# Performance work log

Hardware: AMD Instinct MI355X
Metric: run time of the kernel (lower is better)

## Reference

```python
import jax, jax.numpy as jnp
import numpy as np

TOPK = 6
E = 512
IN = 384
M = 8192
LN_EPS = 1e-5


def _lin(x, w, b):
    # torch nn.Linear: y = x @ W^T + b, W is [out, in]
    return x @ w.T + b


def setup_inputs() -> dict:
    key = jax.random.key(0)
    ks = jax.random.split(key, 16)
    s = lambda k, sh: (jax.random.normal(k, sh, dtype=jnp.float32) * 0.02)
    return {
        "x": jax.random.normal(ks[0], (1, M, IN), dtype=jnp.float32),
        "fc1_w": s(ks[1], (E, IN)), "fc1_b": jnp.zeros((E,), jnp.float32),
        "wh_w": s(ks[2], (E, E)),   "wh_b": jnp.zeros((E,), jnp.float32),
        "wt_w": s(ks[3], (E, E)),   "wt_b": jnp.zeros((E,), jnp.float32),
        "l1_w": s(ks[4], (E, E)),   "l1_b": jnp.zeros((E,), jnp.float32),
        "l2_w": s(ks[5], (E, E)),   "l2_b": jnp.zeros((E,), jnp.float32),
        "a1_w": s(ks[6], (E // 2, E)), "a1_b": jnp.zeros((E // 2,), jnp.float32),
        "a2_w": s(ks[7], (1, E // 2)), "a2_b": jnp.zeros((1,), jnp.float32),
        "ln_g": jnp.ones((E,), jnp.float32), "ln_b": jnp.zeros((E,), jnp.float32),
    }


def reference(x, fc1_w, fc1_b, wh_w, wh_b, wt_w, wt_b,
              l1_w, l1_b, l2_w, l2_b, a1_w, a1_b, a2_w, a2_b, ln_g, ln_b):
    lrelu = jax.nn.leaky_relu  # slope 0.01 == torch default
    h = lrelu(_lin(x, fc1_w, fc1_b))                      # [B,M,E]
    h = (h + h.mean(axis=1, keepdims=True)) * 0.5
    e_h = _lin(h, wh_w, wh_b)                             # [B,M,E]
    e_t = _lin(h, wt_w, wt_b)                             # [B,M,E]
    scale = E ** (-0.5)
    attn_logit = (e_h * scale) @ jnp.swapaxes(e_t, -2, -1)  # [B,M,M]
    topk_weight, topk_index = jax.lax.top_k(attn_logit, TOPK)  # [B,M,K]
    # gather top-k neighbor tail embeddings: [B,M,K,E]
    Nb_h = jax.vmap(lambda et, idx: et[idx])(e_t, topk_index)
    topk_prob = jax.nn.softmax(topk_weight, axis=2)       # [B,M,K]
    eh_r = topk_prob[..., None] * Nb_h + (1.0 - topk_prob)[..., None] * e_h[:, :, None, :]
    gate = jnp.tanh(e_h[:, :, None, :] + eh_r)            # [B,M,K,E]
    # faithful to torch einsum('ijkl,ijkm->ijk'): sums l and m independently
    ka_weight = Nb_h.sum(axis=-1) * gate.sum(axis=-1)     # [B,M,K]
    ka_prob = jax.nn.softmax(ka_weight, axis=2)           # [B,M,K]
    e_Nh = jnp.einsum('bmk,bmke->bme', ka_prob, Nb_h)     # [B,M,E]
    sum_emb = lrelu(_lin(e_h + e_Nh, l1_w, l1_b))
    bi_emb = lrelu(_lin(e_h * e_Nh, l2_w, l2_b))
    emb = sum_emb + bi_emb                                # [B,M,E] (dropout = eval identity)
    hn = emb[0]                                           # squeeze(0) -> [M,E]
    # GeoGlobalAttention readout: gate_nn = Linear->LeakyReLU->Linear, softmax over nodes
    g = _lin(lrelu(_lin(hn, a1_w, a1_b)), a2_w, a2_b)     # [M,1]
    att = jax.nn.softmax(g, axis=0)
    pooled = (att * hn).sum(axis=0, keepdims=True)        # [1,E]
    mu = pooled.mean(axis=-1, keepdims=True)
    var = jnp.mean((pooled - mu) ** 2, axis=-1, keepdims=True)
    out = (pooled - mu) / jnp.sqrt(var + LN_EPS) * ln_g + ln_b
    return out
```

## Files before the change

kernel.cpp:

```cpp
#include <hip/hip_runtime.h>
#include <math.h>
#include <stdint.h>

#define M_NODES 8192
#define E_DIM   512
#define NTOPK   6
#define ATTN_SCALE 0.04419417382415922f
#define NEG_BIG (-1e38f)
#define CAND_CAP 192

typedef __attribute__((ext_vector_type(8))) short short8;
typedef __attribute__((ext_vector_type(4))) float f32x4;

__device__ __forceinline__ float lrelu(float v) { return v > 0.f ? v : 0.01f * v; }

__device__ __forceinline__ unsigned short f2bf(float f) {
  uint32_t u = __float_as_uint(f);
  uint32_t r = (u + 0x7FFFu + ((u >> 16) & 1u)) >> 16;
  return (unsigned short)r;
}
__device__ __forceinline__ float bf2f(unsigned short s) {
  return __uint_as_float(((uint32_t)s) << 16);
}

__device__ __forceinline__ void async_cp16(const void* gptr, void* lds) {
  auto g1 = reinterpret_cast<const __attribute__((address_space(1))) unsigned int*>(
      reinterpret_cast<uintptr_t>(gptr));
  auto l3 = reinterpret_cast<__attribute__((address_space(3))) unsigned int*>(
      reinterpret_cast<uintptr_t>(lds));
  __builtin_amdgcn_global_load_lds(g1, l3, 16, 0, 0);
}



__global__ __launch_bounds__(256) void wcast_kernel(
    const float* __restrict__ x, const float* __restrict__ fc1w,
    const float* __restrict__ whw, const float* __restrict__ wtw,
    const float* __restrict__ l1w, const float* __restrict__ l2w,
    const float* __restrict__ a1w,
    unsigned short* __restrict__ xT, unsigned short* __restrict__ fc1T,
    unsigned short* __restrict__ whT, unsigned short* __restrict__ wtT,
    unsigned short* __restrict__ l1T, unsigned short* __restrict__ l2T,
    unsigned short* __restrict__ a1T)
{
  const int gid = blockIdx.x * 256 + threadIdx.x;
  const float* src; unsigned short* dst; int K8, local;
  if (gid < 417792) {
    K8 = 48;
    if (gid < 393216) { src = x; dst = xT; local = gid; }
    else { src = fc1w; dst = fc1T; local = gid - 393216; }
  } else {
    K8 = 64;
    if (gid < 450560)      { src = whw; dst = whT; local = gid - 417792; }
    else if (gid < 483328) { src = wtw; dst = wtT; local = gid - 450560; }
    else if (gid < 516096) { src = l1w; dst = l1T; local = gid - 483328; }
    else if (gid < 548864) { src = l2w; dst = l2T; local = gid - 516096; }
    else                   { src = a1w; dst = a1T; local = gid - 548864; }
  }
  const int m = local / K8;
  const int k8 = local - m * K8;
  const float* p = src + (size_t)m * (K8 * 8) + k8 * 8;
  float4 v0 = ((const float4*)p)[0];
  float4 v1 = ((const float4*)p)[1];
  const int Kt = K8 >> 2;
  const size_t ti = ((size_t)(m >> 4) * Kt + (k8 >> 2)) * 512 + ((m & 15) + 16 * (k8 & 3)) * 8;
  uint4 pk;
  pk.x = (uint32_t)f2bf(v0.x) | ((uint32_t)f2bf(v0.y) << 16);
  pk.y = (uint32_t)f2bf(v0.z) | ((uint32_t)f2bf(v0.w) << 16);
  pk.z = (uint32_t)f2bf(v1.x) | ((uint32_t)f2bf(v1.y) << 16);
  pk.w = (uint32_t)f2bf(v1.z) | ((uint32_t)f2bf(v1.w) << 16);
  *(uint4*)(dst + ti) = pk;
}

template <int MODE>
__global__ __launch_bounds__(256) void mfma_gemm(
    const unsigned short* __restrict__ At1, const unsigned short* __restrict__ At2,
    const unsigned short* __restrict__ Wt1, const unsigned short* __restrict__ Wt2,
    const float* __restrict__ b1, const float* __restrict__ b2,
    float* __restrict__ Cf, unsigned short* __restrict__ T1,
    unsigned short* __restrict__ T2, unsigned short* __restrict__ Cbf,
    unsigned short* __restrict__ Cbf2, int N, int K)
{
  constexpr bool DUALW = (MODE == 1 || MODE == 2);
  __shared__ unsigned short As[2][8 * 512];
  __shared__ unsigned short Bs[2][4 * 512];
  const int Kt = K >> 5;
  const int tid = threadIdx.x, lane = tid & 63, w = tid >> 6;
  const int m0 = blockIdx.y * 128, n0 = blockIdx.x * 64;

  f32x4 acc0[2][4], acc1[2][4];
#pragma unroll
  for (int p = 0; p < 2; p++)
#pragma unroll
    for (int j = 0; j < 4; j++) {
      acc0[p][j] = (f32x4){0.f, 0.f, 0.f, 0.f};
      acc1[p][j] = (f32x4){0.f, 0.f, 0.f, 0.f};
    }

  for (int kt = 0; kt < Kt; kt++) {
    const unsigned short* a1p = At1 + ((size_t)((m0 >> 4) + 2 * w) * Kt + kt) * 512 + lane * 8;
    async_cp16(a1p, &As[0][(2 * w) * 512]);
    async_cp16(a1p + (size_t)Kt * 512, &As[0][(2 * w + 1) * 512]);
    if (MODE == 2) {
      const unsigned short* a2p = At2 + ((size_t)((m0 >> 4) + 2 * w) * Kt + kt) * 512 + lane * 8;
      async_cp16(a2p, &As[1][(2 * w) * 512]);
      async_cp16(a2p + (size_t)Kt * 512, &As[1][(2 * w + 1) * 512]);
    }
    const unsigned short* bp1 = Wt1 + ((size_t)((n0 >> 4) + w) * Kt + kt) * 512 + lane * 8;
    async_cp16(bp1, &Bs[0][w * 512]);
    if (DUALW) {
      const unsigned short* bp2 = Wt2 + ((size_t)((n0 >> 4) + w) * Kt + kt) * 512 + lane * 8;
      async_cp16(bp2, &Bs[1][w * 512]);
    }
    __syncthreads();
    short8 a[2], a2[2], bb[4], bb2[4];
#pragma unroll
    for (int p = 0; p < 2; p++) a[p] = *(const short8*)&As[0][(2 * w + p) * 512 + lane * 8];
    if (MODE == 2) {
#pragma unroll
      for (int p = 0; p < 2; p++) a2[p] = *(const short8*)&As[1][(2 * w + p) * 512 + lane * 8];
    }
#pragma unroll
    for (int j = 0; j < 4; j++) bb[j] = *(const short8*)&Bs[0][j * 512 + lane * 8];
    if (DUALW) {
#pragma unroll
      for (int j = 0; j < 4; j++) bb2[j] = *(const short8*)&Bs[1][j * 512 + lane * 8];
    }
#pragma unroll
    for (int p = 0; p < 2; p++)
#pragma unroll
      for (int j = 0; j < 4; j++) {
        acc0[p][j] = __builtin_amdgcn_mfma_f32_16x16x32_bf16(a[p], bb[j], acc0[p][j], 0, 0, 0);
        if (MODE == 1)
          acc1[p][j] = __builtin_amdgcn_mfma_f32_16x16x32_bf16(a[p], bb2[j], acc1[p][j], 0, 0, 0);
        if (MODE == 2)
          acc1[p][j] = __builtin_amdgcn_mfma_f32_16x16x32_bf16(a2[p], bb2[j], acc1[p][j], 0, 0, 0);
      }
    __syncthreads();
  }

  const int lrow = (lane >> 4) * 4, lcol = lane & 15;

  if (MODE == 3) {
    float part[2][4] = {};
#pragma unroll
    for (int p = 0; p < 2; p++)
#pragma unroll
      for (int j = 0; j < 4; j++) {
        const int c = n0 + j * 16 + lcol;
        const float bias1 = b1[c];
        const float w2 = b2[c];
#pragma unroll
        for (int d = 0; d < 4; d++)
          part[p][d] = fmaf(lrelu(acc0[p][j][d] + bias1), w2, part[p][d]);
      }
#pragma unroll
    for (int p = 0; p < 2; p++)
#pragma unroll
      for (int d = 0; d < 4; d++) {
#pragma unroll
        for (int off = 1; off < 16; off <<= 1)
          part[p][d] += __shfl_xor(part[p][d], off);
      }
    if (lcol == 0) {
#pragma unroll
      for (int p = 0; p < 2; p++)
#pragma unroll
        for (int d = 0; d < 4; d++)
          atomicAdd(&Cf[m0 + w * 32 + p * 16 + lrow + d], part[p][d]);
    }
    return;
  }

  if (MODE == 4) {
    float colp[4] = {};
#pragma unroll
    for (int p = 0; p < 2; p++)
#pragma unroll
      for (int j = 0; j < 4; j++) {
        const int c = n0 + j * 16 + lcol;
        const float bias1 = b1[c];
#pragma unroll
        for (int d = 0; d < 4; d++) {
          const int r = m0 + w * 32 + p * 16 + lrow + d;
          const float v = lrelu(acc0[p][j][d] + bias1);
          Cbf[(size_t)r * N + c] = f2bf(v);
          colp[j] += v;
        }
      }
#pragma unroll
    for (int j = 0; j < 4; j++) {
      colp[j] += __shfl_xor(colp[j], 16);
      colp[j] += __shfl_xor(colp[j], 32);
    }
    if (lane < 16) {
#pragma unroll
      for (int j = 0; j < 4; j++)
        atomicAdd(&Cf[n0 + j * 16 + lcol], colp[j]);
    }
    return;
  }

  const int NT = N >> 5;
#pragma unroll
  for (int p = 0; p < 2; p++)
#pragma unroll
    for (int j = 0; j < 4; j++) {
      const int c = n0 + j * 16 + lcol;
      const float bias1 = b1[c];
      const float bias2 = DUALW ? b2[c] : 0.f;
#pragma unroll
      for (int d = 0; d < 4; d++) {
        const int r = m0 + w * 32 + p * 16 + lrow + d;
        const float v0 = acc0[p][j][d] + bias1;
        const size_t ti = ((size_t)(r >> 4) * NT + (c >> 5)) * 512 +
                          ((r & 15) + 16 * ((c >> 3) & 3)) * 8 + (c & 7);
        if (MODE == 1) {
          const float v1 = acc1[p][j][d] + bias2;
          T1[ti] = f2bf(v0);
          T2[ti] = f2bf(v1);
          Cbf[(size_t)r * N + c] = f2bf(v0);
          Cbf2[(size_t)r * N + c] = f2bf(v1);
        } else {
          const float e = lrelu(v0) + lrelu(acc1[p][j][d] + bias2);
          T1[ti] = f2bf(e);
          Cbf[(size_t)r * N + c] = f2bf(e);
        }
      }
    }
}

__global__ __launch_bounds__(256) void hupd_cast_kernel(
    const unsigned short* __restrict__ hRow, const float* __restrict__ colsum,
    unsigned short* __restrict__ hT)
{
  const int gid = blockIdx.x * 256 + threadIdx.x;
  const int m = gid >> 6, k8 = gid & 63;
  short8 hv = *(const short8*)(hRow + (size_t)m * E_DIM + k8 * 8);
  float4 c0 = *(const float4*)(colsum + k8 * 8);
  float4 c1 = *(const float4*)(colsum + k8 * 8 + 4);
  const float im = 1.f / (float)M_NODES;
  float v[8];
#pragma unroll
  for (int e = 0; e < 8; e++) v[e] = bf2f((unsigned short)hv[e]);
  v[0] = (v[0] + c0.x * im) * 0.5f; v[1] = (v[1] + c0.y * im) * 0.5f;
  v[2] = (v[2] + c0.z * im) * 0.5f; v[3] = (v[3] + c0.w * im) * 0.5f;
  v[4] = (v[4] + c1.x * im) * 0.5f; v[5] = (v[5] + c1.y * im) * 0.5f;
  v[6] = (v[6] + c1.z * im) * 0.5f; v[7] = (v[7] + c1.w * im) * 0.5f;
  const size_t ti = ((size_t)(m >> 4) * 16 + (k8 >> 2)) * 512 + ((m & 15) + 16 * (k8 & 3)) * 8;
  uint4 pk;
  pk.x = (uint32_t)f2bf(v[0]) | ((uint32_t)f2bf(v[1]) << 16);
  pk.y = (uint32_t)f2bf(v[2]) | ((uint32_t)f2bf(v[3]) << 16);
  pk.z = (uint32_t)f2bf(v[4]) | ((uint32_t)f2bf(v[5]) << 16);
  pk.w = (uint32_t)f2bf(v[6]) | ((uint32_t)f2bf(v[7]) << 16);
  *(uint4*)(hT + ti) = pk;
}

__global__ __launch_bounds__(256, 4) void sgemm_kernel(
    const unsigned short* __restrict__ ehT, const unsigned short* __restrict__ etT,
    unsigned short* __restrict__ sc, float* __restrict__ tmax)
{
  __shared__ unsigned short As[8 * 512];
  __shared__ unsigned short Bs[8 * 512];
  const int tid = threadIdx.x, lane = tid & 63, w = tid >> 6;
  const int wr = w >> 1, wc = w & 1;
  const int m0 = blockIdx.y * 128;
  const int n0 = blockIdx.x * 128;

  f32x4 acc[4][4];
#pragma unroll
  for (int i = 0; i < 4; i++)
#pragma unroll
    for (int j = 0; j < 4; j++) acc[i][j] = (f32x4){0.f, 0.f, 0.f, 0.f};

  for (int kt = 0; kt < 16; kt++) {
    const int s0 = w, s1 = w + 4;
    async_cp16(ehT + ((size_t)((m0 >> 4) + s0) * 16 + kt) * 512 + lane * 8, &As[s0 * 512]);
    async_cp16(ehT + ((size_t)((m0 >> 4) + s1) * 16 + kt) * 512 + lane * 8, &As[s1 * 512]);
    async_cp16(etT + ((size_t)((n0 >> 4) + s0) * 16 + kt) * 512 + lane * 8, &Bs[s0 * 512]);
    async_cp16(etT + ((size_t)((n0 >> 4) + s1) * 16 + kt) * 512 + lane * 8, &Bs[s1 * 512]);
    __syncthreads();
    short8 a[4], b[4];
#pragma unroll
    for (int i = 0; i < 4; i++) a[i] = *(const short8*)&As[(wr * 4 + i) * 512 + lane * 8];
#pragma unroll
    for (int j = 0; j < 4; j++) b[j] = *(const short8*)&Bs[(wc * 4 + j) * 512 + lane * 8];
#pragma unroll
    for (int i = 0; i < 4; i++)
#pragma unroll
      for (int j = 0; j < 4; j++)
        acc[i][j] = __builtin_amdgcn_mfma_f32_16x16x32_bf16(a[i], b[j], acc[i][j], 0, 0, 0);
    __syncthreads();
  }

  const int q = lane >> 4, lcol = lane & 15;
  const int bn = blockIdx.x;

  float rm[4][4];
#pragma unroll
  for (int i = 0; i < 4; i++)
#pragma unroll
    for (int d = 0; d < 4; d++) rm[i][d] = NEG_BIG;

#pragma unroll
  for (int i = 0; i < 4; i++)
#pragma unroll
    for (int d = 0; d < 4; d++) {
      unsigned short o[4];
#pragma unroll
      for (int j = 0; j < 4; j++) {
        o[j] = f2bf(acc[i][j][d]);
        rm[i][d] = fmaxf(rm[i][d], bf2f(o[j]));
      }
      const int row = m0 + wr * 64 + i * 16 + q * 4 + d;
      const size_t off = ((size_t)row * 64 + bn) * 128 + (wc * 16 + lcol) * 4;
      *(uint2*)(sc + off) = *(uint2*)o;
    }

#pragma unroll
  for (int i = 0; i < 4; i++)
#pragma unroll
    for (int d = 0; d < 4; d++) {
#pragma unroll
      for (int off = 1; off < 16; off <<= 1)
        rm[i][d] = fmaxf(rm[i][d], __shfl_xor(rm[i][d], off));
    }

  if (lcol == 0) {
#pragma unroll
    for (int i = 0; i < 4; i++)
#pragma unroll
      for (int d = 0; d < 4; d++)
        tmax[(size_t)(m0 + wr * 64 + i * 16 + q * 4 + d) * 128 +
             bn * 2 + wc] = rm[i][d];
  }
}

__global__ __launch_bounds__(256) void scan_combine_kernel(
    const unsigned short* __restrict__ sc, const float* __restrict__ tmax,
    const unsigned short* __restrict__ ehRow, const unsigned short* __restrict__ etRow,
    unsigned short* __restrict__ s1T, unsigned short* __restrict__ s2T)
{
  __shared__ float cv[4][CAND_CAP];
  __shared__ int   ci[4][CAND_CAP];
  __shared__ int   cnt[4];
  __shared__ float t6v[4][8];
  __shared__ int   t6i[4][8];
  const int tid = threadIdx.x;
  const int lane = tid & 63;
  const int w = tid >> 6;
  const int row = blockIdx.x * 4 + w;

  if (lane == 0) cnt[w] = 0;
  if (lane < 8) { t6v[w][lane] = 0.f; t6i[w][lane] = 0; }

  const float* tm = tmax + (size_t)row * 128;
  const float v2 = fmaxf(tm[lane], tm[lane + 64]);
  const float bmax = fmaxf(tm[2 * lane], tm[2 * lane + 1]);
  uint32_t u = __float_as_uint(v2);
  u = ((int)u >= 0) ? (u | 0x80000000u) : ~u;
  uint32_t key = (u & ~63u) | (uint32_t)lane;
  float tau = 0.f;
#pragma unroll
  for (int it = 0; it < 6; it++) {
    uint32_t k = key;
#pragma unroll
    for (int off = 32; off; off >>= 1) {
      const uint32_t o = (uint32_t)__shfl_xor((int)k, off);
      k = k > o ? k : o;
    }
    const int wl = (int)(k & 63u);
    if (it == 5) tau = __shfl(v2, wl);
    if (lane == wl) key = 0u;
  }

  unsigned long long mask = __ballot(bmax >= tau);
  const unsigned short* rp = sc + (size_t)row * 8192;
  while (mask) {
    const int bn = __ffsll(mask) - 1;
    mask &= mask - 1;
    const uint32_t uu = *(const uint32_t*)(rp + bn * 128 + lane * 2);
    const float f0 = bf2f((unsigned short)(uu & 0xFFFFu));
    const float f1 = bf2f((unsigned short)(uu >> 16));
#pragma unroll
    for (int e = 0; e < 2; e++) {
      const float f = e ? f1 : f0;
      if (f >= tau) {
        const int idx128 = lane * 2 + e;
        const int g = idx128 >> 2, j = idx128 & 3;
        const int col = bn * 128 + (g >> 4) * 64 + j * 16 + (g & 15);
        const int slot = atomicAdd(&cnt[w], 1);
        if (slot < CAND_CAP) { cv[w][slot] = f; ci[w][slot] = col; }
      }
    }
  }
  __syncthreads();

  int n = cnt[w];
  n = n < CAND_CAP ? n : CAND_CAP;
  for (int c = lane; c < n; c += 64) {
    const float v = cv[w][c];
    const int idx = ci[w][c];
    int rank = 0;
    for (int j = 0; j < n; j++) {
      const float vj = cv[w][j];
      rank += (vj > v) || (vj == v && ci[w][j] < idx);
    }
    if (rank < NTOPK) { t6v[w][rank] = v; t6i[w][rank] = idx; }
  }
  __syncthreads();

  const int m = row;
  float wv[NTOPK]; int id[NTOPK];
#pragma unroll
  for (int k = 0; k < NTOPK; k++) {
    wv[k] = t6v[w][k] * ATTN_SCALE;
    id[k] = t6i[w][k];
  }

  float mx = wv[0];
#pragma unroll
  for (int k = 1; k < NTOPK; k++) mx = fmaxf(mx, wv[k]);
  float p[NTOPK]; float s = 0.f;
#pragma unroll
  for (int k = 0; k < NTOPK; k++) { p[k] = expf(wv[k] - mx); s += p[k]; }
  const float inv = 1.f / s;
#pragma unroll
  for (int k = 0; k < NTOPK; k++) p[k] *= inv;

  short8 eh8 = *(const short8*)(ehRow + (size_t)m * E_DIM + lane * 8);
  float ehv[8];
#pragma unroll
  for (int e = 0; e < 8; e++) ehv[e] = bf2f((unsigned short)eh8[e]);

  float nv[NTOPK][8];
#pragma unroll
  for (int k = 0; k < NTOPK; k++) {
    short8 nb = *(const short8*)(etRow + (size_t)id[k] * E_DIM + lane * 8);
#pragma unroll
    for (int e = 0; e < 8; e++) nv[k][e] = bf2f((unsigned short)nb[e]);
  }

  float ka[NTOPK];
#pragma unroll
  for (int k = 0; k < NTOPK; k++) {
    float snb = 0.f, sg = 0.f;
    const float aa = 2.f - p[k], bb = p[k];
#pragma unroll
    for (int e = 0; e < 8; e++) {
      snb += nv[k][e];
      sg += tanhf(fmaf(aa, ehv[e], bb * nv[k][e]));
    }
#pragma unroll
    for (int off = 32; off; off >>= 1) {
      snb += __shfl_xor(snb, off);
      sg += __shfl_xor(sg, off);
    }
    ka[k] = snb * sg;
  }
  float km = ka[0];
#pragma unroll
  for (int k = 1; k < NTOPK; k++) km = fmaxf(km, ka[k]);
  float kp[NTOPK]; float ks = 0.f;
#pragma unroll
  for (int k = 0; k < NTOPK; k++) { kp[k] = expf(ka[k] - km); ks += kp[k]; }
  const float kinv = 1.f / ks;

  const size_t tbase = ((size_t)(m >> 4) * 16 + (lane >> 2)) * 512 +
                       ((m & 15) + 16 * (lane & 3)) * 8;
  unsigned short o1[8], o2[8];
#pragma unroll
  for (int e = 0; e < 8; e++) {
    float o = 0.f;
#pragma unroll
    for (int k = 0; k < NTOPK; k++) o = fmaf(kp[k], nv[k][e], o);
    o *= kinv;
    o1[e] = f2bf(ehv[e] + o);
    o2[e] = f2bf(ehv[e] * o);
  }
  *(short8*)(s1T + tbase) = *(short8*)o1;
  *(short8*)(s2T + tbase) = *(short8*)o2;
}

__global__ __launch_bounds__(256) void pooled_kernel(
    const unsigned short* __restrict__ emb, const float* __restrict__ g,
    float* __restrict__ pooled, float* __restrict__ wsum)
{
  const int t = threadIdx.x;
  const int r0 = blockIdx.x * 128;
  float a0 = 0.f, a1 = 0.f, lsum = 0.f;
  for (int r = 0; r < 128; r++) {
    const int m = r0 + r;
    const float wv = expf(g[m]);
    lsum += wv;
    a0 = fmaf(wv, bf2f(emb[(size_t)m * E_DIM + t]), a0);
    a1 = fmaf(wv, bf2f(emb[(size_t)m * E_DIM + 256 + t]), a1);
  }
  atomicAdd(&pooled[t], a0);
  atomicAdd(&pooled[t + 256], a1);
  if (t == 0) atomicAdd(wsum, lsum);
}

__global__ __launch_bounds__(512) void ln_kernel(
    const float* __restrict__ pooled, const float* __restrict__ wsum,
    const float* __restrict__ lng, const float* __restrict__ lnb,
    float* __restrict__ out)
{
  __shared__ float red[8];
  __shared__ float red2[8];
  const int t = threadIdx.x;
  const float v = pooled[t] / wsum[0];
  float s = v;
#pragma unroll
  for (int off = 32; off; off >>= 1) s += __shfl_xor(s, off);
  if ((t & 63) == 0) red[t >> 6] = s;
  __syncthreads();
  float tot = 0.f;
  for (int i = 0; i < 8; i++) tot += red[i];
  const float mu = tot / (float)E_DIM;
  const float d = v - mu;
  float q = d * d;
#pragma unroll
  for (int off = 32; off; off >>= 1) q += __shfl_xor(q, off);
  if ((t & 63) == 0) red2[t >> 6] = q;
  __syncthreads();
  float vt = 0.f;
  for (int i = 0; i < 8; i++) vt += red2[i];
  const float var = vt / (float)E_DIM;
  out[t] = d * rsqrtf(var + 1e-5f) * lng[t] + lnb[t];
}

extern "C" void kernel_launch(void* const* d_in, const int* in_sizes, int n_in,
                              void* d_out, int out_size, void* d_ws, size_t ws_size,
                              hipStream_t stream)
{
  const float* x     = (const float*)d_in[0];
  const float* fc1_w = (const float*)d_in[1];
  const float* fc1_b = (const float*)d_in[2];
  const float* wh_w  = (const float*)d_in[3];
  const float* wh_b  = (const float*)d_in[4];
  const float* wt_w  = (const float*)d_in[5];
  const float* wt_b  = (const float*)d_in[6];
  const float* l1_w  = (const float*)d_in[7];
  const float* l1_b  = (const float*)d_in[8];
  const float* l2_w  = (const float*)d_in[9];
  const float* l2_b  = (const float*)d_in[10];
  const float* a1_w  = (const float*)d_in[11];
  const float* a1_b  = (const float*)d_in[12];
  const float* a2_w  = (const float*)d_in[13];
  const float* a2_b  = (const float*)d_in[14];
  const float* ln_g  = (const float*)d_in[15];
  const float* ln_b  = (const float*)d_in[16];
  (void)a2_b;

  char* ws = (char*)d_ws;
  const size_t MiB = 1 << 20;
  unsigned short* fc1T = (unsigned short*)(ws + 0);
  unsigned short* whT  = (unsigned short*)(ws + 393216);
  unsigned short* wtT  = (unsigned short*)(ws + 917504);
  unsigned short* l1T  = (unsigned short*)(ws + 1441792);
  unsigned short* l2T  = (unsigned short*)(ws + 1966080);
  unsigned short* a1T  = (unsigned short*)(ws + 2490368);
  unsigned short* xT     = (unsigned short*)(ws + 3 * MiB);
  unsigned short* hRow   = (unsigned short*)(ws + 9 * MiB);
  unsigned short* hT     = (unsigned short*)(ws + 25 * MiB);
  unsigned short* ehT    = (unsigned short*)(ws + 33 * MiB);
  unsigned short* etT    = (unsigned short*)(ws + 41 * MiB);
  unsigned short* ehRow  = (unsigned short*)(ws + 49 * MiB);
  unsigned short* etRow  = (unsigned short*)(ws + 57 * MiB);
  float*          tmaxb  = (float*)(ws + 65 * MiB);
  unsigned short* s1T    = (unsigned short*)(ws + 3 * MiB);
  unsigned short* s2T    = (unsigned short*)(ws + 11 * MiB);
  unsigned short* embT   = (unsigned short*)(ws + 19 * MiB);
  unsigned short* embRow = (unsigned short*)(ws + 27 * MiB);
  unsigned short* scores = (unsigned short*)(ws + 96 * MiB);
  char*           smal   = ws + 69 * MiB;
  float* colsum = (float*)(smal);
  float* g      = (float*)(smal + 4096);
  float* stats  = (float*)(smal + 36864);
  float* pooled = (float*)(smal + 40960);

  hipMemsetAsync(smal, 0, 43008, stream);

  wcast_kernel<<<2208, 256, 0, stream>>>(x, fc1_w, wh_w, wt_w, l1_w, l2_w, a1_w,
                                         xT, fc1T, whT, wtT, l1T, l2T, a1T);
  mfma_gemm<4><<<dim3(8, 64), 256, 0, stream>>>(
      xT, nullptr, fc1T, nullptr, fc1_b, nullptr, colsum, nullptr, nullptr, hRow, nullptr,
      512, 384);
  hupd_cast_kernel<<<2048, 256, 0, stream>>>(hRow, colsum, hT);
  mfma_gemm<1><<<dim3(8, 64), 256, 0, stream>>>(
      hT, nullptr, whT, wtT, wh_b, wt_b, nullptr, ehT, etT, ehRow, etRow, 512, 512);
  sgemm_kernel<<<dim3(64, 64), 256, 0, stream>>>(ehT, etT, scores, tmaxb);
  scan_combine_kernel<<<M_NODES / 4, 256, 0, stream>>>(
      scores, tmaxb, ehRow, etRow, s1T, s2T);
  mfma_gemm<2><<<dim3(8, 64), 256, 0, stream>>>(
      s1T, s2T, l1T, l2T, l1_b, l2_b, nullptr, embT, nullptr, embRow, nullptr, 512, 512);
  mfma_gemm<3><<<dim3(4, 64), 256, 0, stream>>>(
      embT, nullptr, a1T, nullptr, a1_b, a2_w, g, nullptr, nullptr, nullptr, nullptr,
      256, 512);
  pooled_kernel<<<64, 256, 0, stream>>>(embRow, g, pooled, stats);
  ln_kernel<<<1, 512, 0, stream>>>(pooled, stats, ln_g, ln_b, (float*)d_out);
}
```

Baseline: 306.3 us.

## Fold node-mean into projection bias and fuse fc1 output into tiled layout

```diff
diff --git a/kernel.cpp b/kernel.cpp
--- a/kernel.cpp
+++ b/kernel.cpp
@@ -72,16 +72,165 @@
   *(uint4*)(dst + ti) = pk;
 }
 
+__global__ __launch_bounds__(256, 4) void gemm1_kernel(
+    const unsigned short* __restrict__ xT, const unsigned short* __restrict__ fc1T,
+    const float* __restrict__ b1, unsigned short* __restrict__ hT,
+    float* __restrict__ colsum)
+{
+  __shared__ unsigned short As[8 * 512];
+  __shared__ unsigned short Bs[8 * 512];
+  const int tid = threadIdx.x, lane = tid & 63, w = tid >> 6;
+  const int wr = w >> 1, wc = w & 1;
+  const int m0 = blockIdx.y * 128;
+  const int n0 = blockIdx.x * 128;
+
+  f32x4 acc[4][4];
+#pragma unroll
+  for (int i = 0; i < 4; i++)
+#pragma unroll
+    for (int j = 0; j < 4; j++) acc[i][j] = (f32x4){0.f, 0.f, 0.f, 0.f};
+
+  for (int kt = 0; kt < 12; kt++) {
+    const int s0 = w, s1 = w + 4;
+    async_cp16(xT + ((size_t)((m0 >> 4) + s0) * 12 + kt) * 512 + lane * 8, &As[s0 * 512]);
+    async_cp16(xT + ((size_t)((m0 >> 4) + s1) * 12 + kt) * 512 + lane * 8, &As[s1 * 512]);
+    async_cp16(fc1T + ((size_t)((n0 >> 4) + s0) * 12 + kt) * 512 + lane * 8, &Bs[s0 * 512]);
+    async_cp16(fc1T + ((size_t)((n0 >> 4) + s1) * 12 + kt) * 512 + lane * 8, &Bs[s1 * 512]);
+    __syncthreads();
+    short8 a[4], b[4];
+#pragma unroll
+    for (int i = 0; i < 4; i++) a[i] = *(const short8*)&As[(wr * 4 + i) * 512 + lane * 8];
+#pragma unroll
+    for (int j = 0; j < 4; j++) b[j] = *(const short8*)&Bs[(wc * 4 + j) * 512 + lane * 8];
+#pragma unroll
+    for (int i = 0; i < 4; i++)
+#pragma unroll
+      for (int j = 0; j < 4; j++)
+        acc[i][j] = __builtin_amdgcn_mfma_f32_16x16x32_bf16(a[i], b[j], acc[i][j], 0, 0, 0);
+    __syncthreads();
+  }
+
+  const int q = lane >> 4, lcol = lane & 15;
+  float colp[4] = {};
+#pragma unroll
+  for (int i = 0; i < 4; i++)
+#pragma unroll
+    for (int j = 0; j < 4; j++) {
+      const int c = n0 + wc * 64 + j * 16 + lcol;
+      const float bias = b1[c];
+#pragma unroll
+      for (int d = 0; d < 4; d++) {
+        const int r = m0 + wr * 64 + i * 16 + q * 4 + d;
+        const float v = 0.5f * lrelu(acc[i][j][d] + bias);
+        hT[((size_t)(r >> 4) * 16 + (c >> 5)) * 512 +
+           ((r & 15) + 16 * ((c >> 3) & 3)) * 8 + (c & 7)] = f2bf(v);
+        colp[j] += v;
+      }
+    }
+#pragma unroll
+  for (int j = 0; j < 4; j++) {
+    colp[j] += __shfl_xor(colp[j], 16);
+    colp[j] += __shfl_xor(colp[j], 32);
+  }
+  if (lane < 16) {
+#pragma unroll
+    for (int j = 0; j < 4; j++)
+      atomicAdd(&colsum[n0 + wc * 64 + j * 16 + lcol], colp[j]);
+  }
+}
+
+__global__ __launch_bounds__(256) void meanproj_kernel(
+    const float* __restrict__ colsum, const float* __restrict__ whw,
+    const float* __restrict__ wtw, const float* __restrict__ whb,
+    const float* __restrict__ wtb, float* __restrict__ biasHT)
+{
+  const int lane = threadIdx.x & 63;
+  const int c1024 = blockIdx.x * 4 + (threadIdx.x >> 6);
+  const bool isH = c1024 < 512;
+  const int c = isH ? c1024 : c1024 - 512;
+  const float* W = (isH ? whw : wtw) + (size_t)c * 512 + lane * 8;
+  const float* cs = colsum + lane * 8;
+  float s = 0.f;
+#pragma unroll
+  for (int e = 0; e < 8; e++) s = fmaf(cs[e], W[e], s);
+#pragma unroll
+  for (int off = 32; off; off >>= 1) s += __shfl_xor(s, off);
+  if (lane == 0)
+    biasHT[c1024] = (isH ? whb : wtb)[c] + s * (1.f / (float)M_NODES);
+}
+
+__global__ __launch_bounds__(256, 4) void dual_gemm(
+    const unsigned short* __restrict__ hT, const unsigned short* __restrict__ wstackT,
+    const float* __restrict__ biasHT,
+    unsigned short* __restrict__ ehT, unsigned short* __restrict__ etT,
+    unsigned short* __restrict__ ehRow, unsigned short* __restrict__ etRow)
+{
+  __shared__ unsigned short As[8 * 512];
+  __shared__ unsigned short Bs[8 * 512];
+  const int tid = threadIdx.x, lane = tid & 63, w = tid >> 6;
+  const int wr = w >> 1, wc = w & 1;
+  const int m0 = blockIdx.y * 128;
+  const int n0 = blockIdx.x * 128;
+
+  f32x4 acc[4][4];
+#pragma unroll
+  for (int i = 0; i < 4; i++)
+#pragma unroll
+    for (int j = 0; j < 4; j++) acc[i][j] = (f32x4){0.f, 0.f, 0.f, 0.f};
+
+  for (int kt = 0; kt < 16; kt++) {
+    const int s0 = w, s1 = w + 4;
+    async_cp16(hT + ((size_t)((m0 >> 4) + s0) * 16 + kt) * 512 + lane * 8, &As[s0 * 512]);
+    async_cp16(hT + ((size_t)((m0 >> 4) + s1) * 16 + kt) * 512 + lane * 8, &As[s1 * 512]);
+    async_cp16(wstackT + ((size_t)((n0 >> 4) + s0) * 16 + kt) * 512 + lane * 8, &Bs[s0 * 512]);
+    async_cp16(wstackT + ((size_t)((n0 >> 4) + s1) * 16 + kt) * 512 + lane * 8, &Bs[s1 * 512]);
+    __syncthreads();
+    short8 a[4], b[4];
+#pragma unroll
+    for (int i = 0; i < 4; i++) a[i] = *(const short8*)&As[(wr * 4 + i) * 512 + lane * 8];
+#pragma unroll
+    for (int j = 0; j < 4; j++) b[j] = *(const short8*)&Bs[(wc * 4 + j) * 512 + lane * 8];
+#pragma unroll
+    for (int i = 0; i < 4; i++)
+#pragma unroll
+      for (int j = 0; j < 4; j++)
+        acc[i][j] = __builtin_amdgcn_mfma_f32_16x16x32_bf16(a[i], b[j], acc[i][j], 0, 0, 0);
+    __syncthreads();
+  }
+
+  const int q = lane >> 4, lcol = lane & 15;
+  const bool isH = (n0 < 512);
+  const int cb = isH ? n0 : (n0 - 512);
+  unsigned short* T = isH ? ehT : etT;
+  unsigned short* R = isH ? ehRow : etRow;
+
+#pragma unroll
+  for (int i = 0; i < 4; i++)
+#pragma unroll
+    for (int j = 0; j < 4; j++) {
+      const int cl = wc * 64 + j * 16 + lcol;
+      const float bias = biasHT[n0 + cl];
+      const int c = cb + cl;
+#pragma unroll
+      for (int d = 0; d < 4; d++) {
+        const int r = m0 + wr * 64 + i * 16 + q * 4 + d;
+        const unsigned short us = f2bf(acc[i][j][d] + bias);
+        T[((size_t)(r >> 4) * 16 + (c >> 5)) * 512 +
+          ((r & 15) + 16 * ((c >> 3) & 3)) * 8 + (c & 7)] = us;
+        R[(size_t)r * E_DIM + c] = us;
+      }
+    }
+}
+
 template <int MODE>
 __global__ __launch_bounds__(256) void mfma_gemm(
     const unsigned short* __restrict__ At1, const unsigned short* __restrict__ At2,
     const unsigned short* __restrict__ Wt1, const unsigned short* __restrict__ Wt2,
     const float* __restrict__ b1, const float* __restrict__ b2,
     float* __restrict__ Cf, unsigned short* __restrict__ T1,
-    unsigned short* __restrict__ T2, unsigned short* __restrict__ Cbf,
-    unsigned short* __restrict__ Cbf2, int N, int K)
-{
-  constexpr bool DUALW = (MODE == 1 || MODE == 2);
+    unsigned short* __restrict__ Cbf, int N, int K)
+{
+  constexpr bool DUALW = (MODE == 2);
   __shared__ unsigned short As[2][8 * 512];
   __shared__ unsigned short Bs[2][4 * 512];
   const int Kt = K >> 5;
@@ -131,8 +280,6 @@
 #pragma unroll
       for (int j = 0; j < 4; j++) {
         acc0[p][j] = __builtin_amdgcn_mfma_f32_16x16x32_bf16(a[p], bb[j], acc0[p][j], 0, 0, 0);
-        if (MODE == 1)
-          acc1[p][j] = __builtin_amdgcn_mfma_f32_16x16x32_bf16(a[p], bb2[j], acc1[p][j], 0, 0, 0);
         if (MODE == 2)
           acc1[p][j] = __builtin_amdgcn_mfma_f32_16x16x32_bf16(a2[p], bb2[j], acc1[p][j], 0, 0, 0);
       }
@@ -172,35 +319,6 @@
     return;
   }
 
-  if (MODE == 4) {
-    float colp[4] = {};
-#pragma unroll
-    for (int p = 0; p < 2; p++)
-#pragma unroll
-      for (int j = 0; j < 4; j++) {
-        const int c = n0 + j * 16 + lcol;
-        const float bias1 = b1[c];
-#pragma unroll
-        for (int d = 0; d < 4; d++) {
-          const int r = m0 + w * 32 + p * 16 + lrow + d;
-          const float v = lrelu(acc0[p][j][d] + bias1);
-          Cbf[(size_t)r * N + c] = f2bf(v);
-          colp[j] += v;
-        }
-      }
-#pragma unroll
-    for (int j = 0; j < 4; j++) {
-      colp[j] += __shfl_xor(colp[j], 16);
-      colp[j] += __shfl_xor(colp[j], 32);
-    }
-    if (lane < 16) {
-#pragma unroll
-      for (int j = 0; j < 4; j++)
-        atomicAdd(&Cf[n0 + j * 16 + lcol], colp[j]);
-    }
-    return;
-  }
-
   const int NT = N >> 5;
 #pragma unroll
   for (int p = 0; p < 2; p++)
@@ -208,52 +326,16 @@
     for (int j = 0; j < 4; j++) {
       const int c = n0 + j * 16 + lcol;
       const float bias1 = b1[c];
-      const float bias2 = DUALW ? b2[c] : 0.f;
+      const float bias2 = b2[c];
 #pragma unroll
       for (int d = 0; d < 4; d++) {
         const int r = m0 + w * 32 + p * 16 + lrow + d;
-        const float v0 = acc0[p][j][d] + bias1;
-        const size_t ti = ((size_t)(r >> 4) * NT + (c >> 5)) * 512 +
-                          ((r & 15) + 16 * ((c >> 3) & 3)) * 8 + (c & 7);
-        if (MODE == 1) {
-          const float v1 = acc1[p][j][d] + bias2;
-          T1[ti] = f2bf(v0);
-          T2[ti] = f2bf(v1);
-          Cbf[(size_t)r * N + c] = f2bf(v0);
-          Cbf2[(size_t)r * N + c] = f2bf(v1);
-        } else {
-          const float e = lrelu(v0) + lrelu(acc1[p][j][d] + bias2);
-          T1[ti] = f2bf(e);
-          Cbf[(size_t)r * N + c] = f2bf(e);
-        }
-      }
-    }
-}
-
-__global__ __launch_bounds__(256) void hupd_cast_kernel(
-    const unsigned short* __restrict__ hRow, const float* __restrict__ colsum,
-    unsigned short* __restrict__ hT)
-{
-  const int gid = blockIdx.x * 256 + threadIdx.x;
-  const int m = gid >> 6, k8 = gid & 63;
-  short8 hv = *(const short8*)(hRow + (size_t)m * E_DIM + k8 * 8);
-  float4 c0 = *(const float4*)(colsum + k8 * 8);
-  float4 c1 = *(const float4*)(colsum + k8 * 8 + 4);
-  const float im = 1.f / (float)M_NODES;
-  float v[8];
-#pragma unroll
-  for (int e = 0; e < 8; e++) v[e] = bf2f((unsigned short)hv[e]);
-  v[0] = (v[0] + c0.x * im) * 0.5f; v[1] = (v[1] + c0.y * im) * 0.5f;
-  v[2] = (v[2] + c0.z * im) * 0.5f; v[3] = (v[3] + c0.w * im) * 0.5f;
-  v[4] = (v[4] + c1.x * im) * 0.5f; v[5] = (v[5] + c1.y * im) * 0.5f;
-  v[6] = (v[6] + c1.z * im) * 0.5f; v[7] = (v[7] + c1.w * im) * 0.5f;
-  const size_t ti = ((size_t)(m >> 4) * 16 + (k8 >> 2)) * 512 + ((m & 15) + 16 * (k8 & 3)) * 8;
-  uint4 pk;
-  pk.x = (uint32_t)f2bf(v[0]) | ((uint32_t)f2bf(v[1]) << 16);
-  pk.y = (uint32_t)f2bf(v[2]) | ((uint32_t)f2bf(v[3]) << 16);
-  pk.z = (uint32_t)f2bf(v[4]) | ((uint32_t)f2bf(v[5]) << 16);
-  pk.w = (uint32_t)f2bf(v[6]) | ((uint32_t)f2bf(v[7]) << 16);
-  *(uint4*)(hT + ti) = pk;
+        const float e = lrelu(acc0[p][j][d] + bias1) + lrelu(acc1[p][j][d] + bias2);
+        T1[((size_t)(r >> 4) * NT + (c >> 5)) * 512 +
+           ((r & 15) + 16 * ((c >> 3) & 3)) * 8 + (c & 7)] = f2bf(e);
+        Cbf[(size_t)r * N + c] = f2bf(e);
+      }
+    }
 }
 
 __global__ __launch_bounds__(256, 4) void sgemm_kernel(
@@ -562,7 +644,6 @@
   unsigned short* l2T  = (unsigned short*)(ws + 1966080);
   unsigned short* a1T  = (unsigned short*)(ws + 2490368);
   unsigned short* xT     = (unsigned short*)(ws + 3 * MiB);
-  unsigned short* hRow   = (unsigned short*)(ws + 9 * MiB);
   unsigned short* hT     = (unsigned short*)(ws + 25 * MiB);
   unsigned short* ehT    = (unsigned short*)(ws + 33 * MiB);
   unsigned short* etT    = (unsigned short*)(ws + 41 * MiB);
@@ -576,28 +657,25 @@
   unsigned short* scores = (unsigned short*)(ws + 96 * MiB);
   char*           smal   = ws + 69 * MiB;
   float* colsum = (float*)(smal);
-  float* g      = (float*)(smal + 4096);
-  float* stats  = (float*)(smal + 36864);
-  float* pooled = (float*)(smal + 40960);
-
-  hipMemsetAsync(smal, 0, 43008, stream);
+  float* biasHT = (float*)(smal + 2048);
+  float* g      = (float*)(smal + 8192);
+  float* stats  = (float*)(smal + 40960);
+  float* pooled = (float*)(smal + 45056);
+
+  hipMemsetAsync(smal, 0, 47104, stream);
 
   wcast_kernel<<<2208, 256, 0, stream>>>(x, fc1_w, wh_w, wt_w, l1_w, l2_w, a1_w,
                                          xT, fc1T, whT, wtT, l1T, l2T, a1T);
-  mfma_gemm<4><<<dim3(8, 64), 256, 0, stream>>>(
-      xT, nullptr, fc1T, nullptr, fc1_b, nullptr, colsum, nullptr, nullptr, hRow, nullptr,
-      512, 384);
-  hupd_cast_kernel<<<2048, 256, 0, stream>>>(hRow, colsum, hT);
-  mfma_gemm<1><<<dim3(8, 64), 256, 0, stream>>>(
-      hT, nullptr, whT, wtT, wh_b, wt_b, nullptr, ehT, etT, ehRow, etRow, 512, 512);
+  gemm1_kernel<<<dim3(4, 64), 256, 0, stream>>>(xT, fc1T, fc1_b, hT, colsum);
+  meanproj_kernel<<<256, 256, 0, stream>>>(colsum, wh_w, wt_w, wh_b, wt_b, biasHT);
+  dual_gemm<<<dim3(8, 64), 256, 0, stream>>>(hT, whT, biasHT, ehT, etT, ehRow, etRow);
   sgemm_kernel<<<dim3(64, 64), 256, 0, stream>>>(ehT, etT, scores, tmaxb);
   scan_combine_kernel<<<M_NODES / 4, 256, 0, stream>>>(
       scores, tmaxb, ehRow, etRow, s1T, s2T);
   mfma_gemm<2><<<dim3(8, 64), 256, 0, stream>>>(
-      s1T, s2T, l1T, l2T, l1_b, l2_b, nullptr, embT, nullptr, embRow, nullptr, 512, 512);
+      s1T, s2T, l1T, l2T, l1_b, l2_b, nullptr, embT, embRow, 512, 512);
   mfma_gemm<3><<<dim3(4, 64), 256, 0, stream>>>(
-      embT, nullptr, a1T, nullptr, a1_b, a2_w, g, nullptr, nullptr, nullptr, nullptr,
-      256, 512);
+      embT, nullptr, a1T, nullptr, a1_b, a2_w, g, nullptr, nullptr, 256, 512);
   pooled_kernel<<<64, 256, 0, stream>>>(embRow, g, pooled, stats);
   ln_kernel<<<1, 512, 0, stream>>>(pooled, stats, ln_g, ln_b, (float*)d_out);
 }
```

Result: faster. 293.7 us (-4.1%).
